# Performance work log

Hardware: AMD Instinct MI355X
Metric: run time of the kernel (lower is better)

## Reference

```python
import jax, jax.numpy as jnp
import numpy as np

K = 3            # kernel_size
PAD = K // 2
CENTER_OFFSET = 0.0


def obb2offset(obb, stride):
    """obb: [N,5,H,W] (x_ctr,y_ctr,w,h,theta) in image coords -> deform offsets [N,2*K*K,H,W]."""
    N, _, H, W = obb.shape
    idx = jnp.arange(-PAD, PAD + 1, dtype=jnp.float32)
    yy, xx = jnp.meshgrid(idx, idx, indexing='ij')   # torch.meshgrid default 'ij'
    xx = xx.reshape(-1)                               # [KK]
    yy = yy.reshape(-1)
    x_ctr, y_ctr, w, h, a = [obb[:, i] for i in range(5)]   # each [N,H,W]
    s = jnp.float32(stride)
    x_ctr, y_ctr, w, h = x_ctr / s, y_ctr / s, w / s, h / s
    cos, sin = jnp.cos(a), jnp.sin(a)
    dw, dh = w / K, h / K
    px = dw[..., None] * xx                           # [N,H,W,KK]
    py = dh[..., None] * yy
    xr = cos[..., None] * px - sin[..., None] * py    # rotate kernel grid by theta
    yr = sin[..., None] * px + cos[..., None] * py
    x_anchor = xr + x_ctr[..., None]
    y_anchor = yr + y_ctr[..., None]
    xc = jnp.arange(W, dtype=jnp.float32)
    yc = jnp.arange(H, dtype=jnp.float32)
    x_conv = xc[None, None, :, None] + xx + CENTER_OFFSET   # [1,1,W,KK]
    y_conv = yc[None, :, None, None] + yy + CENTER_OFFSET   # [1,H,1,KK]
    off = jnp.stack([y_anchor - y_conv, x_anchor - x_conv], axis=-1)  # [N,H,W,KK,2]
    return off.reshape(N, H, W, 2 * K * K).transpose(0, 3, 1, 2)


def deform_conv(x, offsets, weight):
    """Deformable conv v1, zero padding, stride 1. x:[N,Cin,H,W], offsets:[N,2KK,H,W], weight:[Cout,Cin,K,K]."""
    N, Cin, H, W = x.shape
    KK = K * K
    Cout = weight.shape[0]
    off = offsets.reshape(N, KK, 2, H, W)
    dy, dx = off[:, :, 0], off[:, :, 1]                        # [N,KK,H,W]
    ky = jnp.arange(KK, dtype=jnp.float32) // K - PAD
    kx = jnp.arange(KK, dtype=jnp.float32) % K - PAD
    py = jnp.arange(H, dtype=jnp.float32)[None, None, :, None] + ky[None, :, None, None] + dy
    px = jnp.arange(W, dtype=jnp.float32)[None, None, None, :] + kx[None, :, None, None] + dx
    y0 = jnp.floor(py)
    x0 = jnp.floor(px)
    ly = py - y0                                               # bilinear fractions
    lx = px - x0
    y0i = y0.astype(jnp.int32)
    x0i = x0.astype(jnp.int32)
    x_flat = x.reshape(N, Cin, H * W)

    def corner(iy, ix):
        valid = (iy >= 0) & (iy < H) & (ix >= 0) & (ix < W)
        idx = jnp.clip(iy, 0, H - 1) * W + jnp.clip(ix, 0, W - 1)  # [N,KK,H,W]
        g = jax.vmap(lambda xf, ii: xf[:, ii.reshape(-1)].reshape(Cin, KK, H, W))(x_flat, idx)
        return jnp.where(valid[:, None], g, 0.0)               # [N,Cin,KK,H,W]

    v00 = corner(y0i, x0i)
    v01 = corner(y0i, x0i + 1)
    v10 = corner(y0i + 1, x0i)
    v11 = corner(y0i + 1, x0i + 1)
    wy = ly[:, None]
    wx = lx[:, None]
    sampled = (v00 * (1 - wy) * (1 - wx) + v01 * (1 - wy) * wx
               + v10 * wy * (1 - wx) + v11 * wy * wx)          # [N,Cin,KK,H,W]
    return jnp.einsum('nckhw,ock->nohw', sampled, weight.reshape(Cout, Cin, KK))


def setup_inputs() -> dict:
    key = jax.random.key(0)
    k1, k2, k3, k4, k5, k6 = jax.random.split(key, 6)
    N, Cin, Cout, H, W, stride = 2, 256, 256, 128, 128, 8
    x = jax.random.normal(k1, (N, Cin, H, W), jnp.float32)
    gy, gx = jnp.meshgrid(jnp.arange(H, dtype=jnp.float32), jnp.arange(W, dtype=jnp.float32), indexing='ij')
    xc = (gx[None] + jax.random.uniform(k2, (N, H, W), minval=-0.5, maxval=0.5)) * stride
    yc = (gy[None] + jax.random.uniform(k3, (N, H, W), minval=-0.5, maxval=0.5)) * stride
    wb = jax.random.uniform(k4, (N, H, W), minval=2.0 * stride, maxval=8.0 * stride)
    hb = jax.random.uniform(k5, (N, H, W), minval=2.0 * stride, maxval=8.0 * stride)
    th = jax.random.uniform(k6, (N, H, W), minval=-np.pi / 2, maxval=np.pi / 2)
    obb = jnp.stack([xc, yc, wb, hb, th], axis=1)              # [N,5,H,W]
    weight = jax.random.normal(jax.random.fold_in(key, 7), (Cout, Cin, K, K), jnp.float32) * 0.02
    return {"x": x, "obb": obb, "weight": weight, "stride": stride}


def reference(x, obb, weight, stride):
    offsets = obb2offset(jax.lax.stop_gradient(obb), stride)   # offsets.detach() in original
    return deform_conv(x, offsets, weight)
```

## Files before the change

kernel.cpp:

```cpp
#include <hip/hip_runtime.h>

#define HH 128
#define WW 128
#define CIN 256
#define COUT 256
#define KTOT 2304
#define HW (HH * WW)
#define NIT 36

typedef __attribute__((ext_vector_type(8))) short short8;
typedef __attribute__((ext_vector_type(4))) float f32x4;
typedef __attribute__((ext_vector_type(2))) float f32x2;

__device__ __forceinline__ unsigned rne_bf16(float f) {
  unsigned u = __float_as_uint(f);
  return (u + 0x7FFFu + ((u >> 16) & 1u)) >> 16;
}
__device__ __forceinline__ unsigned pack_bf16x2(float lo, float hi) {
  return rne_bf16(lo) | (rne_bf16(hi) << 16);
}
__device__ __forceinline__ unsigned cvt_pk_bf16(float lo, float hi) {
  unsigned r;
  asm("v_cvt_pk_bf16_f32 %0, %1, %2" : "=v"(r) : "v"(lo), "v"(hi));
  return r;
}
__device__ __forceinline__ f32x2 up2(unsigned u) {
  f32x2 r;
  r.x = __uint_as_float(u << 16);
  r.y = __uint_as_float(u & 0xFFFF0000u);
  return r;
}
__device__ __forceinline__ f32x2 pkmul(f32x2 w, f32x2 v) {
  f32x2 d;
  asm("v_pk_mul_f32 %0, %1, %2" : "=v"(d) : "v"(w), "v"(v));
  return d;
}
__device__ __forceinline__ f32x2 pkfma(f32x2 w, f32x2 v, f32x2 c) {
  f32x2 d;
  asm("v_pk_fma_f32 %0, %1, %2, %3" : "=v"(d) : "v"(w), "v"(v), "v"(c));
  return d;
}

__global__ void prep_inputs(const float* __restrict__ x, const float* __restrict__ wsrc,
                            unsigned short* __restrict__ xt, unsigned short* __restrict__ wB) {
  int b = blockIdx.x;
  __shared__ float tile[64][129];
  if (b < 1024) {
    int cg = b & 3;
    int nh = b >> 2;
    int n = nh >> 7, h = nh & 127;
    int c0 = cg << 6;
    const float* xp = x + ((size_t)n * CIN * HH + h) * WW;
    for (int e = threadIdx.x; e < 64 * 128; e += 256) {
      int w = e & 127, ci = e >> 7;
      tile[ci][w] = xp[(size_t)(c0 + ci) * HW + w];
    }
    __syncthreads();
    unsigned* dst = (unsigned*)(xt + ((size_t)(n * HH + h) * WW) * CIN + c0);
    for (int e = threadIdx.x; e < 128 * 32; e += 256) {
      int w = e >> 5, cp = e & 31;
      dst[w * (CIN / 2) + cp] = pack_bf16x2(tile[2 * cp][w], tile[2 * cp + 1][w]);
    }
  } else {
    int o = (b - 1024) * 256 + threadIdx.x;
    if (o >= COUT * KTOT) return;
    int co = o / KTOT;
    int r = o - co * KTOT;
    int kk = r >> 8, ci = r & 255;
    int it = r >> 6;
    int rem = r & 63;
    int ksi = rem >> 5;
    int l4 = (rem >> 3) & 3;
    int e = rem & 7;
    int off = (it * 32 + (co >> 4) * 2 + ksi) * 512 + (l4 * 16 + (co & 15)) * 8 + e;
    wB[off] = rne_bf16(wsrc[(size_t)(co * CIN + ci) * 9 + kk]);
  }
}

__global__ __launch_bounds__(512, 4) void fused_deform_gemm(
    const float* __restrict__ obb, const unsigned short* __restrict__ xt,
    const unsigned short* __restrict__ wB, float* __restrict__ out,
    const int* __restrict__ stride_p) {
  int g = blockIdx.x;
  int xcd = g & 7, li = g >> 3;
  int u = xcd * 64 + li;
  int mh = u & 1;
  int bm = u >> 1;
  int n = bm >> 7, h = bm & 127;
  int tid = threadIdx.x;

  __shared__ __align__(16) unsigned short Alds[2][64 * 64];

  float inv_s = 1.0f / (float)stride_p[0];

  int lane = tid & 63;
  int wv = tid >> 6;
  int wm = (wv & 1) * 32;
  int wn = (wv >> 1) * 64;
  int l15 = lane & 15, l4 = lane >> 4;

  int chunk8 = (lane & 7) * 8;
  int p = wv * 8 + (lane >> 3);
  int AldsOff = p * 128 + (((lane & 7) * 16) ^ ((p & 7) << 4));

  float cx_, cy_, pa_, pb_, pc_, pd_;
  {
    int w = mh * 64 + p;
    const float* op = obb + ((size_t)n * 5 * HH + h) * WW + w;
    float xc = op[0] * inv_s;
    float yc = op[(size_t)1 * HW] * inv_s;
    float bw = op[(size_t)2 * HW] * inv_s;
    float bh = op[(size_t)3 * HW] * inv_s;
    float th = op[(size_t)4 * HW];
    float sn, cs;
    sincosf(th, &sn, &cs);
    float dw = bw * (1.0f / 3.0f), dh = bh * (1.0f / 3.0f);
    cx_ = xc; cy_ = yc;
    pa_ = dw * cs; pb_ = dh * sn;
    pc_ = dw * sn; pd_ = dh * cs;
  }

  f32x4 acc[2][4] = {};

  const char* wBb = (const char*)wB + ((wv >> 1) * 4) * 2048 + lane * 16;

  int rdXor = (l15 & 7) << 4;
  int rc0 = (l4 * 16) ^ rdXor;
  int rc1 = (64 + l4 * 16) ^ rdXor;

  f32x2 wgt2[4];
  int boff[4];
  uint4 pf[4];
  uint4 aw;

  auto prep = [&](int kk) {
    float fky = (float)(kk / 3 - 1);
    float fkx = (float)(kk % 3 - 1);
    float sx = cx_ + fkx * pa_ - fky * pb_;
    float sy = cy_ + fkx * pc_ + fky * pd_;
    float fx = floorf(sx), fy = floorf(sy);
    float lx = sx - fx, ly = sy - fy;
    int x0 = (int)fx, y0 = (int)fy;
    float vy0 = (y0 >= 0 && y0 < HH) ? 1.0f : 0.0f;
    float vy1 = (y0 >= -1 && y0 < HH - 1) ? 1.0f : 0.0f;
    float vx0 = (x0 >= 0 && x0 < WW) ? 1.0f : 0.0f;
    float vx1 = (x0 >= -1 && x0 < WW - 1) ? 1.0f : 0.0f;
    float w00 = (1.0f - ly) * (1.0f - lx) * vy0 * vx0;
    float w01 = (1.0f - ly) * lx * vy0 * vx1;
    float w10 = ly * (1.0f - lx) * vy1 * vx0;
    float w11 = ly * lx * vy1 * vx1;
    wgt2[0] = (f32x2){w00, w00};
    wgt2[1] = (f32x2){w01, w01};
    wgt2[2] = (f32x2){w10, w10};
    wgt2[3] = (f32x2){w11, w11};
    int xc0 = min(max(x0, 0), WW - 1), xc1 = min(max(x0 + 1, 0), WW - 1);
    int yc0 = min(max(y0, 0), HH - 1), yc1 = min(max(y0 + 1, 0), HH - 1);
    int rb0 = (n * HH + yc0) * WW, rb1 = (n * HH + yc1) * WW;
    boff[0] = (rb0 + xc0) * CIN;
    boff[1] = (rb0 + xc1) * CIN;
    boff[2] = (rb1 + xc0) * CIN;
    boff[3] = (rb1 + xc1) * CIN;
  };

  auto issueA = [&](int cc) {
    int co = cc * 64 + chunk8;
#pragma unroll
    for (int c = 0; c < 4; ++c)
      pf[c] = *(const uint4*)(xt + boff[c] + co);
  };

  auto blendW = [&](unsigned a, unsigned b, unsigned c, unsigned d) -> unsigned {
    f32x2 s = pkmul(wgt2[0], up2(a));
    s = pkfma(wgt2[1], up2(b), s);
    s = pkfma(wgt2[2], up2(c), s);
    s = pkfma(wgt2[3], up2(d), s);
    return cvt_pk_bf16(s.x, s.y);
  };

  auto blendA = [&]() {
    uint4 r;
    r.x = blendW(pf[0].x, pf[1].x, pf[2].x, pf[3].x);
    r.y = blendW(pf[0].y, pf[1].y, pf[2].y, pf[3].y);
    r.z = blendW(pf[0].z, pf[1].z, pf[2].z, pf[3].z);
    r.w = blendW(pf[0].w, pf[1].w, pf[2].w, pf[3].w);
    aw = r;
  };

  char* AB = (char*)&Alds[0][0];

  prep(0);
  issueA(0);
  blendA();
  *(uint4*)(AB + AldsOff) = aw;
  issueA(1);
  asm volatile("s_waitcnt lgkmcnt(0)" ::: "memory");
  __builtin_amdgcn_s_barrier();
  asm volatile("" ::: "memory");

  for (int it = 0; it < NIT; ++it) {
    const char* bp = wBb + it * 32768;
    short8 bf[8];
#pragma unroll
    for (int j = 0; j < 4; ++j) {
      bf[j * 2 + 0] = *(const short8*)(bp + j * 2048);
      bf[j * 2 + 1] = *(const short8*)(bp + j * 2048 + 1024);
    }

    if (it + 1 < NIT) {
      blendA();
      *(uint4*)(AB + ((it + 1) & 1) * 8192 + AldsOff) = aw;
      int t2 = it + 2;
      if (t2 < NIT) {
        if ((t2 & 3) == 0) prep(t2 >> 2);
        issueA(t2 & 3);
      }
    }

    char* ABr = AB + (it & 1) * 8192;
    __builtin_amdgcn_s_setprio(1);
#pragma unroll
    for (int ksi = 0; ksi < 2; ++ksi) {
      int rc = ksi ? rc1 : rc0;
      short8 af[2];
#pragma unroll
      for (int i = 0; i < 2; ++i)
        af[i] = *(const short8*)(ABr + (wm + i * 16 + l15) * 128 + rc);
#pragma unroll
      for (int j = 0; j < 4; ++j)
#pragma unroll
        for (int i = 0; i < 2; ++i)
          acc[i][j] = __builtin_amdgcn_mfma_f32_16x16x32_bf16(af[i], bf[j * 2 + ksi], acc[i][j], 0, 0, 0);
    }
    __builtin_amdgcn_s_setprio(0);

    asm volatile("s_waitcnt lgkmcnt(0)" ::: "memory");
    __builtin_amdgcn_s_barrier();
    asm volatile("" ::: "memory");
  }

  float* outp = out + (size_t)n * COUT * HW + (size_t)h * WW + mh * 64;
#pragma unroll
  for (int i = 0; i < 2; ++i) {
    int w0 = wm + i * 16 + l4 * 4;
#pragma unroll
    for (int j = 0; j < 4; ++j) {
      int co = wn + j * 16 + l15;
      *(f32x4*)(outp + (size_t)co * HW + w0) = acc[i][j];
    }
  }
}

extern "C" void kernel_launch(void* const* d_in, const int* in_sizes, int n_in,
                              void* d_out, int out_size, void* d_ws, size_t ws_size,
                              hipStream_t stream) {
  const float* x = (const float*)d_in[0];
  const float* obb = (const float*)d_in[1];
  const float* wgt = (const float*)d_in[2];
  const int* stridep = (const int*)d_in[3];
  float* out = (float*)d_out;

  unsigned short* xt = (unsigned short*)d_ws;
  unsigned short* wB = xt + (size_t)2 * HH * WW * CIN;

  prep_inputs<<<dim3(1024 + 2304), 256, 0, stream>>>(x, wgt, xt, wB);
  fused_deform_gemm<<<dim3(512), 512, 0, stream>>>(obb, xt, wB, out, stridep);
}
```

Measured before the change: 167.4 us.

## Prefetch weight fragments one iteration ahead and vectorize input prep transposes

The GEMM loop now keeps the B-operand register fragments loaded for the next k-iteration, issued in between the MFMAs of the current one, so weight-load latency no longer stalls the start of each iteration. The A fragments for both k-substeps are read from shared memory up front. The prep kernel is reworked to use float4 global loads, a transposed shared tile with vectorized bf16 packing via v_cvt_pk_bf16, and packed two-element weight conversion, which halves the weight-prep grid. These changes add register pressure from the persistent bf array and change the prep kernel's tiling.

```diff
diff --git a/kernel.cpp b/kernel.cpp
--- a/kernel.cpp
+++ b/kernel.cpp
@@ -16,9 +16,6 @@
   unsigned u = __float_as_uint(f);
   return (u + 0x7FFFu + ((u >> 16) & 1u)) >> 16;
 }
-__device__ __forceinline__ unsigned pack_bf16x2(float lo, float hi) {
-  return rne_bf16(lo) | (rne_bf16(hi) << 16);
-}
 __device__ __forceinline__ unsigned cvt_pk_bf16(float lo, float hi) {
   unsigned r;
   asm("v_cvt_pk_bf16_f32 %0, %1, %2" : "=v"(r) : "v"(lo), "v"(hi));
@@ -44,25 +41,40 @@
 __global__ void prep_inputs(const float* __restrict__ x, const float* __restrict__ wsrc,
                             unsigned short* __restrict__ xt, unsigned short* __restrict__ wB) {
   int b = blockIdx.x;
-  __shared__ float tile[64][129];
-  if (b < 1024) {
-    int cg = b & 3;
-    int nh = b >> 2;
+  __shared__ __align__(16) float tile[64][68];
+  int tid = threadIdx.x;
+  if (b < 2048) {
+    int wg = b & 1, cg = (b >> 1) & 3, nh = b >> 3;
     int n = nh >> 7, h = nh & 127;
-    int c0 = cg << 6;
-    const float* xp = x + ((size_t)n * CIN * HH + h) * WW;
-    for (int e = threadIdx.x; e < 64 * 128; e += 256) {
-      int w = e & 127, ci = e >> 7;
-      tile[ci][w] = xp[(size_t)(c0 + ci) * HW + w];
+    const float* xp = x + (((size_t)n * CIN + cg * 64) * HH + h) * WW + wg * 64;
+#pragma unroll
+    for (int r = 0; r < 4; ++r) {
+      int e = r * 256 + tid;
+      int ci = e >> 4, w4 = (e & 15) * 4;
+      float4 v = *(const float4*)(xp + (size_t)ci * HW + w4);
+      tile[w4 + 0][ci] = v.x;
+      tile[w4 + 1][ci] = v.y;
+      tile[w4 + 2][ci] = v.z;
+      tile[w4 + 3][ci] = v.w;
     }
     __syncthreads();
-    unsigned* dst = (unsigned*)(xt + ((size_t)(n * HH + h) * WW) * CIN + c0);
-    for (int e = threadIdx.x; e < 128 * 32; e += 256) {
-      int w = e >> 5, cp = e & 31;
-      dst[w * (CIN / 2) + cp] = pack_bf16x2(tile[2 * cp][w], tile[2 * cp + 1][w]);
+    unsigned short* dst = xt + (((size_t)(n * HH + h) * WW) + wg * 64) * CIN + cg * 64;
+#pragma unroll
+    for (int r = 0; r < 2; ++r) {
+      int e = r * 256 + tid;
+      int w = e >> 3, c8 = (e & 7) * 8;
+      const float* tp = &tile[w][c8];
+      f32x4 lo = *(const f32x4*)tp;
+      f32x4 hi = *(const f32x4*)(tp + 4);
+      uint4 o;
+      o.x = cvt_pk_bf16(lo.x, lo.y);
+      o.y = cvt_pk_bf16(lo.z, lo.w);
+      o.z = cvt_pk_bf16(hi.x, hi.y);
+      o.w = cvt_pk_bf16(hi.z, hi.w);
+      *(uint4*)(dst + (size_t)w * CIN + c8) = o;
     }
   } else {
-    int o = (b - 1024) * 256 + threadIdx.x;
+    int o = (b - 2048) * 512 + tid * 2;
     if (o >= COUT * KTOT) return;
     int co = o / KTOT;
     int r = o - co * KTOT;
@@ -73,7 +85,9 @@
     int l4 = (rem >> 3) & 3;
     int e = rem & 7;
     int off = (it * 32 + (co >> 4) * 2 + ksi) * 512 + (l4 * 16 + (co & 15)) * 8 + e;
-    wB[off] = rne_bf16(wsrc[(size_t)(co * CIN + ci) * 9 + kk]);
+    float v0 = wsrc[(size_t)(co * CIN + ci) * 9 + kk];
+    float v1 = wsrc[(size_t)(co * CIN + ci + 1) * 9 + kk];
+    *(unsigned*)(wB + off) = cvt_pk_bf16(v0, v1);
   }
 }
 
@@ -122,7 +136,7 @@
 
   f32x4 acc[2][4] = {};
 
-  const char* wBb = (const char*)wB + ((wv >> 1) * 4) * 2048 + lane * 16;
+  const char* wBb = (const char*)wB + (wv >> 1) * 8192 + lane * 16;
 
   int rdXor = (l15 & 7) << 4;
   int rc0 = (l4 * 16) ^ rdXor;
@@ -132,6 +146,7 @@
   int boff[4];
   uint4 pf[4];
   uint4 aw;
+  short8 bf[8];
 
   auto prep = [&](int kk) {
     float fky = (float)(kk / 3 - 1);
@@ -192,20 +207,17 @@
   issueA(0);
   blendA();
   *(uint4*)(AB + AldsOff) = aw;
+#pragma unroll
+  for (int j = 0; j < 4; ++j) {
+    bf[j * 2 + 0] = *(const short8*)(wBb + j * 2048);
+    bf[j * 2 + 1] = *(const short8*)(wBb + j * 2048 + 1024);
+  }
   issueA(1);
   asm volatile("s_waitcnt lgkmcnt(0)" ::: "memory");
   __builtin_amdgcn_s_barrier();
   asm volatile("" ::: "memory");
 
   for (int it = 0; it < NIT; ++it) {
-    const char* bp = wBb + it * 32768;
-    short8 bf[8];
-#pragma unroll
-    for (int j = 0; j < 4; ++j) {
-      bf[j * 2 + 0] = *(const short8*)(bp + j * 2048);
-      bf[j * 2 + 1] = *(const short8*)(bp + j * 2048 + 1024);
-    }
-
     if (it + 1 < NIT) {
       blendA();
       *(uint4*)(AB + ((it + 1) & 1) * 8192 + AldsOff) = aw;
@@ -217,19 +229,25 @@
     }
 
     char* ABr = AB + (it & 1) * 8192;
-    __builtin_amdgcn_s_setprio(1);
+    short8 af[2][2];
 #pragma unroll
     for (int ksi = 0; ksi < 2; ++ksi) {
       int rc = ksi ? rc1 : rc0;
-      short8 af[2];
 #pragma unroll
       for (int i = 0; i < 2; ++i)
-        af[i] = *(const short8*)(ABr + (wm + i * 16 + l15) * 128 + rc);
-#pragma unroll
-      for (int j = 0; j < 4; ++j)
-#pragma unroll
-        for (int i = 0; i < 2; ++i)
-          acc[i][j] = __builtin_amdgcn_mfma_f32_16x16x32_bf16(af[i], bf[j * 2 + ksi], acc[i][j], 0, 0, 0);
+        af[ksi][i] = *(const short8*)(ABr + (wm + i * 16 + l15) * 128 + rc);
+    }
+    const char* bpn = wBb + (size_t)((it + 1 < NIT) ? it + 1 : it) * 32768;
+    __builtin_amdgcn_s_setprio(1);
+#pragma unroll
+    for (int j = 0; j < 4; ++j) {
+      short8 b0 = bf[j * 2 + 0], b1 = bf[j * 2 + 1];
+      acc[0][j] = __builtin_amdgcn_mfma_f32_16x16x32_bf16(af[0][0], b0, acc[0][j], 0, 0, 0);
+      acc[1][j] = __builtin_amdgcn_mfma_f32_16x16x32_bf16(af[0][1], b0, acc[1][j], 0, 0, 0);
+      acc[0][j] = __builtin_amdgcn_mfma_f32_16x16x32_bf16(af[1][0], b1, acc[0][j], 0, 0, 0);
+      acc[1][j] = __builtin_amdgcn_mfma_f32_16x16x32_bf16(af[1][1], b1, acc[1][j], 0, 0, 0);
+      bf[j * 2 + 0] = *(const short8*)(bpn + j * 2048);
+      bf[j * 2 + 1] = *(const short8*)(bpn + j * 2048 + 1024);
     }
     __builtin_amdgcn_s_setprio(0);
 
@@ -262,6 +280,6 @@
   unsigned short* xt = (unsigned short*)d_ws;
   unsigned short* wB = xt + (size_t)2 * HH * WW * CIN;
 
-  prep_inputs<<<dim3(1024 + 2304), 256, 0, stream>>>(x, wgt, xt, wB);
+  prep_inputs<<<dim3(2048 + 1152), 256, 0, stream>>>(x, wgt, xt, wB);
   fused_deform_gemm<<<dim3(512), 512, 0, stream>>>(obb, xt, wB, out, stridep);
 }
```

Measured after the change: 200.9 us. 1.2x slower.
